# Performance work log

Measured on AMD Instinct MI355X. Metric: run time of the kernel, lower is better.

The kernel has to match this reference:

```python
import jax, jax.numpy as jnp
import numpy as np


def setup_inputs() -> dict:
    key = jax.random.key(0)
    ks = jax.random.split(key, 8)
    B, D, H, W = 4, 96, 64, 64
    K, N, R = 4, 16, 6
    return {
        "x": jax.random.normal(ks[0], (B, D, H, W), jnp.float32),
        "x_proj_weight": jax.random.normal(ks[1], (K, R + 2 * N, D), jnp.float32) * 0.05,
        "dt_projs_weight": jax.random.normal(ks[2], (K, D, R), jnp.float32) * 0.1,
        "dt_projs_bias": jax.random.normal(ks[3], (K, D), jnp.float32) * 0.1,
        "A_logs": jax.random.uniform(ks[4], (K * D, N), jnp.float32),
        "Ds": jax.random.normal(ks[5], (K * D,), jnp.float32),
        "ln_weight": jnp.ones((D,), jnp.float32),
        "ln_bias": jnp.zeros((D,), jnp.float32),
    }


def reference(x, x_proj_weight, dt_projs_weight, dt_projs_bias, A_logs, Ds, ln_weight, ln_bias):
    B, D, H, W = x.shape
    K, _, R = dt_projs_weight.shape
    N = A_logs.shape[1]
    L = H * W

    # ---- CrossScan: 4 traversal orders (row-major, col-major, and their reverses) ----
    xf = x.reshape(B, D, L)                                   # row-major
    xt = jnp.transpose(x, (0, 1, 3, 2)).reshape(B, D, L)      # col-major
    xs = jnp.stack([xf, xt, xf[..., ::-1], xt[..., ::-1]], axis=1)  # (B, K, D, L)

    # ---- input-dependent projections ----
    x_dbl = jnp.einsum('bkdl,kcd->bkcl', xs, x_proj_weight)   # (B, K, R+2N, L)
    dts, Bs, Cs = jnp.split(x_dbl, [R, R + N], axis=2)        # Bs/Cs: (B, K, N, L)
    dts = jnp.einsum('bkrl,kdr->bkdl', dts, dt_projs_weight)  # (B, K, D, L)

    A = -jnp.exp(A_logs).reshape(K, D, N)                     # (K, D, N)
    delta = jax.nn.softplus(dts + dt_projs_bias[None, :, :, None])  # (B, K, D, L)

    # ---- selective (S6) scan over L ----
    def step(h, inp):
        d_t, u_t, B_t, C_t = inp  # (B,K,D) (B,K,D) (B,K,N) (B,K,N)
        dA = jnp.exp(d_t[..., None] * A[None])                # (B,K,D,N)
        h = h * dA + (d_t * u_t)[..., None] * B_t[:, :, None, :]
        y_t = jnp.einsum('bkdn,bkn->bkd', h, C_t)
        return h, y_t

    h0 = jnp.zeros((B, K, D, N), x.dtype)
    seq = (jnp.moveaxis(delta, -1, 0), jnp.moveaxis(xs, -1, 0),
           jnp.moveaxis(Bs, -1, 0), jnp.moveaxis(Cs, -1, 0))
    _, ys = jax.lax.scan(step, h0, seq)                       # (L, B, K, D)
    ys = jnp.moveaxis(ys, 0, -1)                              # (B, K, D, L)
    ys = ys + Ds.reshape(K, D)[None, :, :, None] * xs         # skip term D*u

    # ---- CrossMerge: undo the 4 traversal orders and sum ----
    m = ys[:, 0:2] + ys[:, 2:4][..., ::-1]                    # (B, 2, D, L)
    y = m[:, 0] + jnp.transpose(m[:, 1].reshape(B, D, W, H), (0, 1, 3, 2)).reshape(B, D, L)

    # ---- out_norm (LayerNorm over channels, v0 path) ----
    y = jnp.transpose(y, (0, 2, 1))                           # (B, L, D)
    mu = y.mean(-1, keepdims=True)
    var = y.var(-1, keepdims=True)
    y = (y - mu) / jnp.sqrt(var + 1e-5) * ln_weight + ln_bias
    return y.reshape(B, H, W, D)
```

## Files before the change

### kernel.cpp

```cpp
#include <hip/hip_runtime.h>
#include <math.h>

#define B_ 4
#define D_ 96
#define H_ 64
#define W_ 64
#define L_ 4096
#define K_ 4
#define N_ 16
#define R_ 6
#define C_ 38
#define S_ 64
#define CL_ (L_ / S_)
#define CH_ (B_ * K_ * D_ * N_)

__device__ __forceinline__ int src_idx(int k, int l) {
    int m = (k >= 2) ? (L_ - 1 - l) : l;
    if (k & 1) {
        return ((m & 63) << 6) | (m >> 6);
    }
    return m;
}

__device__ __forceinline__ float softplus_f(float a) {
    return (a > 15.f) ? a : __logf(1.f + __expf(a));
}

__global__ __launch_bounds__(256) void proj_kernel(
    const float* __restrict__ x,
    const float* __restrict__ xpw,
    const float* __restrict__ wdt,
    const float* __restrict__ bdt,
    float* __restrict__ delta,
    float* __restrict__ xs_t,
    float* __restrict__ Bsb,
    float* __restrict__ Csb)
{
    const int TL = 64;
    const int tiles = L_ / TL;
    int bid = blockIdx.x;
    int bk = bid / tiles;
    int tile = bid % tiles;
    int b = bk / K_, k = bk % K_;
    int l0 = tile * TL;
    int tid = threadIdx.x;

    __shared__ __align__(16) float s_wpT[D_ * 40];
    __shared__ __align__(16) float s_xs[D_ * TL];
    __shared__ __align__(16) float s_wdt[R_ * D_];
    __shared__ __align__(16) float s_bias[D_];
    __shared__ __align__(16) float s_dts[R_ * 68];

    for (int i = tid; i < C_ * D_; i += 256) {
        int d = i / C_, c = i % C_;
        int cp = (c < 6) ? c : c + 2;
        s_wpT[d * 40 + cp] = xpw[(k * C_ + c) * D_ + d];
    }
    for (int i = tid; i < 96; i += 256) {
        s_wpT[i * 40 + 6] = 0.f;
        s_wpT[i * 40 + 7] = 0.f;
    }
    for (int i = tid; i < R_ * D_; i += 256) {
        int r = i / D_, d = i % D_;
        s_wdt[i] = wdt[(k * D_ + d) * R_ + r];
    }
    if (tid < D_) s_bias[tid] = bdt[k * D_ + tid];

    long base = (long)bk * L_ + l0;
    if (k & 1) {
        for (int i = tid; i < D_ * TL; i += 256) {
            int d = i >> 6, lt = i & 63;
            int src = (k == 1) ? (lt * 64 + tile) : ((63 - lt) * 64 + (63 - tile));
            s_xs[d * TL + lt] = x[(b * D_ + d) * L_ + src];
        }
    } else {
        for (int i = tid; i < D_ * 16; i += 256) {
            int d = i >> 4, q = i & 15;
            if (k == 0) {
                float4 v = *(const float4*)(x + (b * D_ + d) * L_ + l0 + q * 4);
                *(float4*)(&s_xs[d * TL + q * 4]) = v;
            } else {
                float4 v = *(const float4*)(x + (b * D_ + d) * L_ + (4092 - l0 - q * 4));
                *(float4*)(&s_xs[d * TL + q * 4]) = make_float4(v.w, v.z, v.y, v.x);
            }
        }
    }

    for (int i = tid; i < 24 * TL; i += 256) {
        int dq = i % 24, lt = i / 24;
        int d0 = dq * 4;
        int src = src_idx(k, l0 + lt);
        const float* xp = x + (long)b * D_ * L_ + src;
        float4 v = make_float4(xp[(d0 + 0) * L_], xp[(d0 + 1) * L_],
                               xp[(d0 + 2) * L_], xp[(d0 + 3) * L_]);
        *(float4*)(&xs_t[(base + lt) * D_ + d0]) = v;
    }
    __syncthreads();

    int ct = tid >> 4;
    int lt4 = (tid & 15) * 4;
    if (ct < 10) {
        int cp0 = ct * 4;
        float acc[4][4];
#pragma unroll
        for (int i = 0; i < 4; ++i)
#pragma unroll
            for (int j = 0; j < 4; ++j) acc[i][j] = 0.f;
#pragma unroll 4
        for (int d = 0; d < D_; ++d) {
            float4 wv = *(const float4*)(&s_wpT[d * 40 + cp0]);
            float4 xv = *(const float4*)(&s_xs[d * TL + lt4]);
            float wa[4] = {wv.x, wv.y, wv.z, wv.w};
            float xa[4] = {xv.x, xv.y, xv.z, xv.w};
#pragma unroll
            for (int ci = 0; ci < 4; ++ci)
#pragma unroll
                for (int li = 0; li < 4; ++li)
                    acc[ci][li] += wa[ci] * xa[li];
        }
        if (ct == 0) {
#pragma unroll
            for (int ci = 0; ci < 4; ++ci)
                *(float4*)(&s_dts[ci * 68 + lt4]) =
                    make_float4(acc[ci][0], acc[ci][1], acc[ci][2], acc[ci][3]);
        } else if (ct == 1) {
#pragma unroll
            for (int ci = 0; ci < 2; ++ci)
                *(float4*)(&s_dts[(4 + ci) * 68 + lt4]) =
                    make_float4(acc[ci][0], acc[ci][1], acc[ci][2], acc[ci][3]);
        } else if (ct < 6) {
            int n0 = cp0 - 8;
#pragma unroll
            for (int li = 0; li < 4; ++li)
                *(float4*)(&Bsb[(base + lt4 + li) * N_ + n0]) =
                    make_float4(acc[0][li], acc[1][li], acc[2][li], acc[3][li]);
        } else {
            int n0 = cp0 - 24;
#pragma unroll
            for (int li = 0; li < 4; ++li)
                *(float4*)(&Csb[(base + lt4 + li) * N_ + n0]) =
                    make_float4(acc[0][li], acc[1][li], acc[2][li], acc[3][li]);
        }
    }
    __syncthreads();

    for (int tt = tid; tt < 24 * 16; tt += 256) {
        int dt = tt % 24, lt4b = (tt / 24) * 4;
        int d0 = dt * 4;
        float4 bias = *(const float4*)(&s_bias[d0]);
        float acc[4][4];
#pragma unroll
        for (int li = 0; li < 4; ++li) {
            acc[li][0] = bias.x; acc[li][1] = bias.y;
            acc[li][2] = bias.z; acc[li][3] = bias.w;
        }
#pragma unroll
        for (int r = 0; r < R_; ++r) {
            float4 wv = *(const float4*)(&s_wdt[r * D_ + d0]);
            float4 tv = *(const float4*)(&s_dts[r * 68 + lt4b]);
            float wa[4] = {wv.x, wv.y, wv.z, wv.w};
            float ta[4] = {tv.x, tv.y, tv.z, tv.w};
#pragma unroll
            for (int li = 0; li < 4; ++li)
#pragma unroll
                for (int di = 0; di < 4; ++di)
                    acc[li][di] += ta[li] * wa[di];
        }
#pragma unroll
        for (int li = 0; li < 4; ++li) {
            float4 o = make_float4(softplus_f(acc[li][0]), softplus_f(acc[li][1]),
                                   softplus_f(acc[li][2]), softplus_f(acc[li][3]));
            *(float4*)(&delta[(base + lt4b + li) * D_ + d0]) = o;
        }
    }
}

__global__ __launch_bounds__(192) void scan_part1(
    const float* __restrict__ A_logs,
    const float* __restrict__ delta,
    const float* __restrict__ xs_t,
    const float* __restrict__ Bsb,
    float* __restrict__ pAarr,
    float* __restrict__ hharr)
{
    int bid = blockIdx.x;
    int bk = bid / S_;
    int j = bid % S_;
    int tid = threadIdx.x;
    int dd = tid >> 1;
    int half = tid & 1;
    int n0 = half * 8;
    int k = bk % K_;
    int kd = k * D_ + dd;
    int l0 = j * CL_;

    float Av[8];
    {
        const float4* ap = (const float4*)(A_logs + kd * N_ + n0);
        float4 a0 = ap[0], a1 = ap[1];
        Av[0] = -__expf(a0.x); Av[1] = -__expf(a0.y);
        Av[2] = -__expf(a0.z); Av[3] = -__expf(a0.w);
        Av[4] = -__expf(a1.x); Av[5] = -__expf(a1.y);
        Av[6] = -__expf(a1.z); Av[7] = -__expf(a1.w);
    }

    const float* dp = delta + ((long)bk * L_ + l0) * D_ + dd;
    const float* up = xs_t + ((long)bk * L_ + l0) * D_ + dd;
    const float* bp = Bsb + ((long)bk * L_ + l0) * N_ + n0;

    float h[8], pA[8];
#pragma unroll
    for (int i = 0; i < 8; ++i) { h[i] = 0.f; pA[i] = 1.f; }

#pragma unroll 4
    for (int t = 0; t < CL_; ++t) {
        float del = dp[t * D_];
        float u   = up[t * D_];
        float4 b0 = *(const float4*)(bp + t * N_);
        float4 b1 = *(const float4*)(bp + t * N_ + 4);
        float Bv[8] = {b0.x, b0.y, b0.z, b0.w, b1.x, b1.y, b1.z, b1.w};
        float delu = del * u;
#pragma unroll
        for (int i = 0; i < 8; ++i) {
            float dA = __expf(del * Av[i]);
            pA[i] *= dA;
            h[i] = h[i] * dA + delu * Bv[i];
        }
    }

    long sbase = (long)j * CH_ + (long)(bk * D_ + dd) * N_ + n0;
    *(float4*)(pAarr + sbase)     = make_float4(pA[0], pA[1], pA[2], pA[3]);
    *(float4*)(pAarr + sbase + 4) = make_float4(pA[4], pA[5], pA[6], pA[7]);
    *(float4*)(hharr + sbase)     = make_float4(h[0], h[1], h[2], h[3]);
    *(float4*)(hharr + sbase + 4) = make_float4(h[4], h[5], h[6], h[7]);
}

__global__ __launch_bounds__(256) void scan_combine(
    const float* __restrict__ pAarr,
    float* __restrict__ hharr)
{
    int c = blockIdx.x * 256 + threadIdx.x;
    float h = 0.f;
#pragma unroll 8
    for (int j = 0; j < S_; ++j) {
        long idx = (long)j * CH_ + c;
        float tmp = hharr[idx];
        float pa  = pAarr[idx];
        hharr[idx] = h;
        h = tmp + pa * h;
    }
}

__global__ __launch_bounds__(192) void scan_part2(
    const float* __restrict__ A_logs,
    const float* __restrict__ Ds,
    const float* __restrict__ delta,
    const float* __restrict__ xs_t,
    const float* __restrict__ Bsb,
    const float* __restrict__ Csb,
    const float* __restrict__ hharr,
    float* __restrict__ ys)
{
    int bid = blockIdx.x;
    int bk = bid / S_;
    int j = bid % S_;
    int tid = threadIdx.x;
    int dd = tid >> 1;
    int half = tid & 1;
    int n0 = half * 8;
    int k = bk % K_;
    int kd = k * D_ + dd;
    int l0 = j * CL_;

    float Av[8];
    {
        const float4* ap = (const float4*)(A_logs + kd * N_ + n0);
        float4 a0 = ap[0], a1 = ap[1];
        Av[0] = -__expf(a0.x); Av[1] = -__expf(a0.y);
        Av[2] = -__expf(a0.z); Av[3] = -__expf(a0.w);
        Av[4] = -__expf(a1.x); Av[5] = -__expf(a1.y);
        Av[6] = -__expf(a1.z); Av[7] = -__expf(a1.w);
    }
    float Dv = Ds[kd];

    const float* dp = delta + ((long)bk * L_ + l0) * D_ + dd;
    const float* up = xs_t + ((long)bk * L_ + l0) * D_ + dd;
    const float* bp = Bsb + ((long)bk * L_ + l0) * N_ + n0;
    const float* cp = Csb + ((long)bk * L_ + l0) * N_ + n0;
    float* yp = ys + ((long)bk * L_ + l0) * D_ + dd;

    float h[8];
    {
        long sbase = (long)j * CH_ + (long)(bk * D_ + dd) * N_ + n0;
        float4 h0 = *(const float4*)(hharr + sbase);
        float4 h1 = *(const float4*)(hharr + sbase + 4);
        h[0] = h0.x; h[1] = h0.y; h[2] = h0.z; h[3] = h0.w;
        h[4] = h1.x; h[5] = h1.y; h[6] = h1.z; h[7] = h1.w;
    }

#pragma unroll 4
    for (int t = 0; t < CL_; ++t) {
        float del = dp[t * D_];
        float u   = up[t * D_];
        float4 b0 = *(const float4*)(bp + t * N_);
        float4 b1 = *(const float4*)(bp + t * N_ + 4);
        float4 c0 = *(const float4*)(cp + t * N_);
        float4 c1 = *(const float4*)(cp + t * N_ + 4);
        float Bv[8] = {b0.x, b0.y, b0.z, b0.w, b1.x, b1.y, b1.z, b1.w};
        float Cv[8] = {c0.x, c0.y, c0.z, c0.w, c1.x, c1.y, c1.z, c1.w};
        float delu = del * u;
        float y = 0.f;
#pragma unroll
        for (int i = 0; i < 8; ++i) {
            float dA = __expf(del * Av[i]);
            h[i] = h[i] * dA + delu * Bv[i];
            y += h[i] * Cv[i];
        }
        y += __shfl_xor(y, 1);
        if (half == 0) yp[t * D_] = y + Dv * u;
    }
}

__global__ __launch_bounds__(64) void scan_serial(
    const float* __restrict__ x,
    const float* __restrict__ A_logs,
    const float* __restrict__ Ds,
    const float* __restrict__ delta,
    const float* __restrict__ Bsb,
    const float* __restrict__ Csb,
    float* __restrict__ ys)
{
    const int chans = D_ / 4;
    int bid = blockIdx.x;
    int bk = bid / chans;
    int d0 = (bid % chans) * 4;
    int b = bk / K_, k = bk % K_;
    int lane = threadIdx.x;
    int g = lane >> 4, n = lane & 15;
    int d = d0 + g;
    int kd = k * D_ + d;

    float A  = -__expf(A_logs[kd * N_ + n]);
    float Dv = Ds[kd];
    const float* dptr = delta + ((long)bk * L_) * D_ + d;
    const float* bptr = Bsb + (long)bk * L_ * N_ + n;
    const float* cptr = Csb + (long)bk * L_ * N_ + n;
    const float* xptr = x + ((long)b * D_ + d) * L_;
    float* yptr = ys + ((long)bk * L_) * D_ + d;

    float h = 0.f;
#pragma unroll 4
    for (int l = 0; l < L_; ++l) {
        float del = dptr[(long)l * D_];
        float u   = xptr[src_idx(k, l)];
        float Bt  = bptr[l * N_];
        float Ct  = cptr[l * N_];
        float dA  = __expf(del * A);
        h = h * dA + del * u * Bt;
        float yv = h * Ct;
        yv += __shfl_xor(yv, 1);
        yv += __shfl_xor(yv, 2);
        yv += __shfl_xor(yv, 4);
        yv += __shfl_xor(yv, 8);
        if (n == 0) yptr[(long)l * D_] = yv + Dv * u;
    }
}

__global__ __launch_bounds__(256) void merge_ln_kernel(
    const float* __restrict__ ys,
    const float* __restrict__ lnw,
    const float* __restrict__ lnb,
    float* __restrict__ out)
{
    int wid = (blockIdx.x * 256 + threadIdx.x) >> 6;
    int lane = threadIdx.x & 63;
    int b = wid / L_;
    int l = wid % L_;
    int lt = ((l & 63) << 6) | (l >> 6);

    long base0 = ((long)(b * K_ + 0) * L_ + l) * D_;
    long base2 = ((long)(b * K_ + 2) * L_ + (L_ - 1 - l)) * D_;
    long base1 = ((long)(b * K_ + 1) * L_ + lt) * D_;
    long base3 = ((long)(b * K_ + 3) * L_ + (L_ - 1 - lt)) * D_;

    int dA = lane;
    int dB = lane + 64;
    float v0 = ys[base0 + dA] + ys[base2 + dA] + ys[base1 + dA] + ys[base3 + dA];
    float v1 = 0.f;
    if (dB < D_)
        v1 = ys[base0 + dB] + ys[base2 + dB] + ys[base1 + dB] + ys[base3 + dB];

    float s  = v0 + v1;
    float s2 = v0 * v0 + v1 * v1;
#pragma unroll
    for (int m = 1; m < 64; m <<= 1) {
        s  += __shfl_xor(s, m);
        s2 += __shfl_xor(s2, m);
    }
    float mu  = s * (1.f / D_);
    float var = s2 * (1.f / D_) - mu * mu;
    float rstd = rsqrtf(var + 1e-5f);

    long obase = ((long)b * L_ + l) * D_;
    out[obase + dA] = (v0 - mu) * rstd * lnw[dA] + lnb[dA];
    if (dB < D_)
        out[obase + dB] = (v1 - mu) * rstd * lnw[dB] + lnb[dB];
}

extern "C" void kernel_launch(void* const* d_in, const int* in_sizes, int n_in,
                              void* d_out, int out_size, void* d_ws, size_t ws_size,
                              hipStream_t stream) {
    const float* x      = (const float*)d_in[0];
    const float* xpw    = (const float*)d_in[1];
    const float* wdt    = (const float*)d_in[2];
    const float* bdt    = (const float*)d_in[3];
    const float* A_logs = (const float*)d_in[4];
    const float* Ds     = (const float*)d_in[5];
    const float* lnw    = (const float*)d_in[6];
    const float* lnb    = (const float*)d_in[7];
    float* out = (float*)d_out;

    float* ws = (float*)d_ws;
    const long n_delta = (long)B_ * K_ * L_ * D_;
    const long n_bc    = (long)B_ * K_ * L_ * N_;
    const long n_sum   = (long)S_ * CH_;
    float* delta = ws;
    float* xs_t  = delta + n_delta;
    float* Bsb   = xs_t + n_delta;
    float* Csb   = Bsb + n_bc;
    float* ys    = Csb + n_bc;
    float* hharr = ys + n_delta;
    float* pAarr = ys;
    size_t need = (size_t)(n_delta * 3 + n_bc * 2 + n_sum) * sizeof(float);

    if (ws_size >= need) {
        proj_kernel<<<B_ * K_ * (L_ / 64), 256, 0, stream>>>(
            x, xpw, wdt, bdt, delta, xs_t, Bsb, Csb);
        scan_part1<<<B_ * K_ * S_, 192, 0, stream>>>(
            A_logs, delta, xs_t, Bsb, pAarr, hharr);
        scan_combine<<<CH_ / 256, 256, 0, stream>>>(pAarr, hharr);
        scan_part2<<<B_ * K_ * S_, 192, 0, stream>>>(
            A_logs, Ds, delta, xs_t, Bsb, Csb, hharr, ys);
        merge_ln_kernel<<<(B_ * L_) / 4, 256, 0, stream>>>(ys, lnw, lnb, out);
    } else {
        float* ys2 = Csb + n_bc;
        proj_kernel<<<B_ * K_ * (L_ / 64), 256, 0, stream>>>(
            x, xpw, wdt, bdt, delta, xs_t, Bsb, Csb);
        scan_serial<<<B_ * K_ * (D_ / 4), 64, 0, stream>>>(
            x, A_logs, Ds, delta, Bsb, Csb, ys2);
        merge_ln_kernel<<<(B_ * L_) / 4, 256, 0, stream>>>(ys2, lnw, lnb, out);
    }
}
```

Measured before the change: 198.2 us.

## Fuse cross-merge into scan via atomics, one thread per channel, more chunks

```diff
diff --git a/kernel.cpp b/kernel.cpp
--- a/kernel.cpp
+++ b/kernel.cpp
@@ -10,8 +10,6 @@
 #define N_ 16
 #define R_ 6
 #define C_ 38
-#define S_ 64
-#define CL_ (L_ / S_)
 #define CH_ (B_ * K_ * D_ * N_)
 
 __device__ __forceinline__ int src_idx(int k, int l) {
@@ -46,7 +44,7 @@
     int tid = threadIdx.x;
 
     __shared__ __align__(16) float s_wpT[D_ * 40];
-    __shared__ __align__(16) float s_xs[D_ * TL];
+    __shared__ __align__(16) float s_xs[D_ * 68];
     __shared__ __align__(16) float s_wdt[R_ * D_];
     __shared__ __align__(16) float s_bias[D_];
     __shared__ __align__(16) float s_dts[R_ * 68];
@@ -71,31 +69,29 @@
         for (int i = tid; i < D_ * TL; i += 256) {
             int d = i >> 6, lt = i & 63;
             int src = (k == 1) ? (lt * 64 + tile) : ((63 - lt) * 64 + (63 - tile));
-            s_xs[d * TL + lt] = x[(b * D_ + d) * L_ + src];
+            s_xs[d * 68 + lt] = x[(b * D_ + d) * L_ + src];
         }
     } else {
         for (int i = tid; i < D_ * 16; i += 256) {
             int d = i >> 4, q = i & 15;
             if (k == 0) {
                 float4 v = *(const float4*)(x + (b * D_ + d) * L_ + l0 + q * 4);
-                *(float4*)(&s_xs[d * TL + q * 4]) = v;
+                *(float4*)(&s_xs[d * 68 + q * 4]) = v;
             } else {
                 float4 v = *(const float4*)(x + (b * D_ + d) * L_ + (4092 - l0 - q * 4));
-                *(float4*)(&s_xs[d * TL + q * 4]) = make_float4(v.w, v.z, v.y, v.x);
+                *(float4*)(&s_xs[d * 68 + q * 4]) = make_float4(v.w, v.z, v.y, v.x);
             }
         }
     }
-
-    for (int i = tid; i < 24 * TL; i += 256) {
-        int dq = i % 24, lt = i / 24;
+    __syncthreads();
+
+    for (int idx = tid; idx < 24 * TL; idx += 256) {
+        int dq = idx % 24, lt = idx / 24;
         int d0 = dq * 4;
-        int src = src_idx(k, l0 + lt);
-        const float* xp = x + (long)b * D_ * L_ + src;
-        float4 v = make_float4(xp[(d0 + 0) * L_], xp[(d0 + 1) * L_],
-                               xp[(d0 + 2) * L_], xp[(d0 + 3) * L_]);
+        float4 v = make_float4(s_xs[(d0 + 0) * 68 + lt], s_xs[(d0 + 1) * 68 + lt],
+                               s_xs[(d0 + 2) * 68 + lt], s_xs[(d0 + 3) * 68 + lt]);
         *(float4*)(&xs_t[(base + lt) * D_ + d0]) = v;
     }
-    __syncthreads();
 
     int ct = tid >> 4;
     int lt4 = (tid & 15) * 4;
@@ -109,7 +105,7 @@
 #pragma unroll 4
         for (int d = 0; d < D_; ++d) {
             float4 wv = *(const float4*)(&s_wpT[d * 40 + cp0]);
-            float4 xv = *(const float4*)(&s_xs[d * TL + lt4]);
+            float4 xv = *(const float4*)(&s_xs[d * 68 + lt4]);
             float wa[4] = {wv.x, wv.y, wv.z, wv.w};
             float xa[4] = {xv.x, xv.y, xv.z, xv.w};
 #pragma unroll
@@ -175,6 +171,7 @@
     }
 }
 
+template <int SS>
 __global__ __launch_bounds__(192) void scan_part1(
     const float* __restrict__ A_logs,
     const float* __restrict__ delta,
@@ -183,58 +180,63 @@
     float* __restrict__ pAarr,
     float* __restrict__ hharr)
 {
-    int bid = blockIdx.x;
-    int bk = bid / S_;
-    int j = bid % S_;
-    int tid = threadIdx.x;
-    int dd = tid >> 1;
-    int half = tid & 1;
-    int n0 = half * 8;
+    constexpr int CLS = L_ / SS;
+    int cid = blockIdx.x * 2 + threadIdx.x / 96;
+    int dd = threadIdx.x % 96;
+    int bk = cid / SS;
+    int j = cid % SS;
     int k = bk % K_;
     int kd = k * D_ + dd;
-    int l0 = j * CL_;
-
-    float Av[8];
+    int l0 = j * CLS;
+
+    float Av[16];
     {
-        const float4* ap = (const float4*)(A_logs + kd * N_ + n0);
-        float4 a0 = ap[0], a1 = ap[1];
-        Av[0] = -__expf(a0.x); Av[1] = -__expf(a0.y);
-        Av[2] = -__expf(a0.z); Av[3] = -__expf(a0.w);
-        Av[4] = -__expf(a1.x); Av[5] = -__expf(a1.y);
-        Av[6] = -__expf(a1.z); Av[7] = -__expf(a1.w);
+        const float4* ap = (const float4*)(A_logs + kd * N_);
+#pragma unroll
+        for (int q = 0; q < 4; ++q) {
+            float4 a = ap[q];
+            Av[q * 4 + 0] = -__expf(a.x); Av[q * 4 + 1] = -__expf(a.y);
+            Av[q * 4 + 2] = -__expf(a.z); Av[q * 4 + 3] = -__expf(a.w);
+        }
     }
 
     const float* dp = delta + ((long)bk * L_ + l0) * D_ + dd;
     const float* up = xs_t + ((long)bk * L_ + l0) * D_ + dd;
-    const float* bp = Bsb + ((long)bk * L_ + l0) * N_ + n0;
-
-    float h[8], pA[8];
-#pragma unroll
-    for (int i = 0; i < 8; ++i) { h[i] = 0.f; pA[i] = 1.f; }
-
-#pragma unroll 4
-    for (int t = 0; t < CL_; ++t) {
+    const float* bp = Bsb + ((long)bk * L_ + l0) * N_;
+
+    float h[16], pA[16];
+#pragma unroll
+    for (int i = 0; i < 16; ++i) { h[i] = 0.f; pA[i] = 1.f; }
+
+#pragma unroll 2
+    for (int t = 0; t < CLS; ++t) {
         float del = dp[t * D_];
         float u   = up[t * D_];
-        float4 b0 = *(const float4*)(bp + t * N_);
-        float4 b1 = *(const float4*)(bp + t * N_ + 4);
-        float Bv[8] = {b0.x, b0.y, b0.z, b0.w, b1.x, b1.y, b1.z, b1.w};
+        float Bv[16];
+        *(float4*)(Bv + 0)  = *(const float4*)(bp + t * N_);
+        *(float4*)(Bv + 4)  = *(const float4*)(bp + t * N_ + 4);
+        *(float4*)(Bv + 8)  = *(const float4*)(bp + t * N_ + 8);
+        *(float4*)(Bv + 12) = *(const float4*)(bp + t * N_ + 12);
         float delu = del * u;
 #pragma unroll
-        for (int i = 0; i < 8; ++i) {
+        for (int i = 0; i < 16; ++i) {
             float dA = __expf(del * Av[i]);
             pA[i] *= dA;
             h[i] = h[i] * dA + delu * Bv[i];
         }
     }
 
-    long sbase = (long)j * CH_ + (long)(bk * D_ + dd) * N_ + n0;
-    *(float4*)(pAarr + sbase)     = make_float4(pA[0], pA[1], pA[2], pA[3]);
-    *(float4*)(pAarr + sbase + 4) = make_float4(pA[4], pA[5], pA[6], pA[7]);
-    *(float4*)(hharr + sbase)     = make_float4(h[0], h[1], h[2], h[3]);
-    *(float4*)(hharr + sbase + 4) = make_float4(h[4], h[5], h[6], h[7]);
-}
-
+    long sbase = (long)j * CH_ + (long)(bk * D_ + dd) * N_;
+#pragma unroll
+    for (int q = 0; q < 4; ++q) {
+        *(float4*)(pAarr + sbase + q * 4) =
+            make_float4(pA[q * 4], pA[q * 4 + 1], pA[q * 4 + 2], pA[q * 4 + 3]);
+        *(float4*)(hharr + sbase + q * 4) =
+            make_float4(h[q * 4], h[q * 4 + 1], h[q * 4 + 2], h[q * 4 + 3]);
+    }
+}
+
+template <int SS>
 __global__ __launch_bounds__(256) void scan_combine(
     const float* __restrict__ pAarr,
     float* __restrict__ hharr)
@@ -242,7 +244,7 @@
     int c = blockIdx.x * 256 + threadIdx.x;
     float h = 0.f;
 #pragma unroll 8
-    for (int j = 0; j < S_; ++j) {
+    for (int j = 0; j < SS; ++j) {
         long idx = (long)j * CH_ + c;
         float tmp = hharr[idx];
         float pa  = pAarr[idx];
@@ -251,6 +253,7 @@
     }
 }
 
+template <int SS>
 __global__ __launch_bounds__(192) void scan_part2(
     const float* __restrict__ A_logs,
     const float* __restrict__ Ds,
@@ -259,66 +262,98 @@
     const float* __restrict__ Bsb,
     const float* __restrict__ Csb,
     const float* __restrict__ hharr,
-    float* __restrict__ ys)
-{
-    int bid = blockIdx.x;
-    int bk = bid / S_;
-    int j = bid % S_;
-    int tid = threadIdx.x;
-    int dd = tid >> 1;
-    int half = tid & 1;
-    int n0 = half * 8;
-    int k = bk % K_;
+    float* __restrict__ y)
+{
+    constexpr int CLS = L_ / SS;
+    int cid = blockIdx.x * 2 + threadIdx.x / 96;
+    int dd = threadIdx.x % 96;
+    int bk = cid / SS;
+    int j = cid % SS;
+    int b = bk / K_, k = bk % K_;
     int kd = k * D_ + dd;
-    int l0 = j * CL_;
-
-    float Av[8];
+    int l0 = j * CLS;
+
+    float Av[16];
     {
-        const float4* ap = (const float4*)(A_logs + kd * N_ + n0);
-        float4 a0 = ap[0], a1 = ap[1];
-        Av[0] = -__expf(a0.x); Av[1] = -__expf(a0.y);
-        Av[2] = -__expf(a0.z); Av[3] = -__expf(a0.w);
-        Av[4] = -__expf(a1.x); Av[5] = -__expf(a1.y);
-        Av[6] = -__expf(a1.z); Av[7] = -__expf(a1.w);
+        const float4* ap = (const float4*)(A_logs + kd * N_);
+#pragma unroll
+        for (int q = 0; q < 4; ++q) {
+            float4 a = ap[q];
+            Av[q * 4 + 0] = -__expf(a.x); Av[q * 4 + 1] = -__expf(a.y);
+            Av[q * 4 + 2] = -__expf(a.z); Av[q * 4 + 3] = -__expf(a.w);
+        }
     }
     float Dv = Ds[kd];
 
     const float* dp = delta + ((long)bk * L_ + l0) * D_ + dd;
     const float* up = xs_t + ((long)bk * L_ + l0) * D_ + dd;
-    const float* bp = Bsb + ((long)bk * L_ + l0) * N_ + n0;
-    const float* cp = Csb + ((long)bk * L_ + l0) * N_ + n0;
-    float* yp = ys + ((long)bk * L_ + l0) * D_ + dd;
-
-    float h[8];
+    const float* bp = Bsb + ((long)bk * L_ + l0) * N_;
+    const float* cp = Csb + ((long)bk * L_ + l0) * N_;
+
+    float h[16];
     {
-        long sbase = (long)j * CH_ + (long)(bk * D_ + dd) * N_ + n0;
-        float4 h0 = *(const float4*)(hharr + sbase);
-        float4 h1 = *(const float4*)(hharr + sbase + 4);
-        h[0] = h0.x; h[1] = h0.y; h[2] = h0.z; h[3] = h0.w;
-        h[4] = h1.x; h[5] = h1.y; h[6] = h1.z; h[7] = h1.w;
-    }
-
-#pragma unroll 4
-    for (int t = 0; t < CL_; ++t) {
+        long sbase = (long)j * CH_ + (long)(bk * D_ + dd) * N_;
+#pragma unroll
+        for (int q = 0; q < 4; ++q) {
+            float4 hv = *(const float4*)(hharr + sbase + q * 4);
+            h[q * 4] = hv.x; h[q * 4 + 1] = hv.y; h[q * 4 + 2] = hv.z; h[q * 4 + 3] = hv.w;
+        }
+    }
+
+    float* ybase = y + (long)b * L_ * D_ + dd;
+#pragma unroll 2
+    for (int t = 0; t < CLS; ++t) {
         float del = dp[t * D_];
         float u   = up[t * D_];
-        float4 b0 = *(const float4*)(bp + t * N_);
-        float4 b1 = *(const float4*)(bp + t * N_ + 4);
-        float4 c0 = *(const float4*)(cp + t * N_);
-        float4 c1 = *(const float4*)(cp + t * N_ + 4);
-        float Bv[8] = {b0.x, b0.y, b0.z, b0.w, b1.x, b1.y, b1.z, b1.w};
-        float Cv[8] = {c0.x, c0.y, c0.z, c0.w, c1.x, c1.y, c1.z, c1.w};
+        float Bv[16], Cv[16];
+        *(float4*)(Bv + 0)  = *(const float4*)(bp + t * N_);
+        *(float4*)(Bv + 4)  = *(const float4*)(bp + t * N_ + 4);
+        *(float4*)(Bv + 8)  = *(const float4*)(bp + t * N_ + 8);
+        *(float4*)(Bv + 12) = *(const float4*)(bp + t * N_ + 12);
+        *(float4*)(Cv + 0)  = *(const float4*)(cp + t * N_);
+        *(float4*)(Cv + 4)  = *(const float4*)(cp + t * N_ + 4);
+        *(float4*)(Cv + 8)  = *(const float4*)(cp + t * N_ + 8);
+        *(float4*)(Cv + 12) = *(const float4*)(cp + t * N_ + 12);
         float delu = del * u;
-        float y = 0.f;
-#pragma unroll
-        for (int i = 0; i < 8; ++i) {
+        float yv = 0.f;
+#pragma unroll
+        for (int i = 0; i < 16; ++i) {
             float dA = __expf(del * Av[i]);
             h[i] = h[i] * dA + delu * Bv[i];
-            y += h[i] * Cv[i];
-        }
-        y += __shfl_xor(y, 1);
-        if (half == 0) yp[t * D_] = y + Dv * u;
-    }
+            yv += h[i] * Cv[i];
+        }
+        int sidx = src_idx(k, l0 + t);
+        atomicAdd(ybase + (long)sidx * D_, yv + Dv * u);
+    }
+}
+
+__global__ __launch_bounds__(256) void ln_kernel(
+    const float* __restrict__ y,
+    const float* __restrict__ lnw,
+    const float* __restrict__ lnb,
+    float* __restrict__ out)
+{
+    int wid = (blockIdx.x * 256 + threadIdx.x) >> 6;
+    int lane = threadIdx.x & 63;
+    long base = (long)wid * D_;
+
+    float v0 = y[base + lane];
+    float v1 = (lane < 32) ? y[base + 64 + lane] : 0.f;
+
+    float s  = v0 + v1;
+    float s2 = v0 * v0 + v1 * v1;
+#pragma unroll
+    for (int m = 1; m < 64; m <<= 1) {
+        s  += __shfl_xor(s, m);
+        s2 += __shfl_xor(s2, m);
+    }
+    float mu  = s * (1.f / D_);
+    float var = s2 * (1.f / D_) - mu * mu;
+    float rstd = rsqrtf(var + 1e-5f);
+
+    out[base + lane] = (v0 - mu) * rstd * lnw[lane] + lnb[lane];
+    if (lane < 32)
+        out[base + 64 + lane] = (v1 - mu) * rstd * lnw[64 + lane] + lnb[64 + lane];
 }
 
 __global__ __launch_bounds__(64) void scan_serial(
@@ -423,27 +458,41 @@
     float* ws = (float*)d_ws;
     const long n_delta = (long)B_ * K_ * L_ * D_;
     const long n_bc    = (long)B_ * K_ * L_ * N_;
-    const long n_sum   = (long)S_ * CH_;
+    const long n_y     = (long)B_ * L_ * D_;
+
     float* delta = ws;
     float* xs_t  = delta + n_delta;
     float* Bsb   = xs_t + n_delta;
     float* Csb   = Bsb + n_bc;
-    float* ys    = Csb + n_bc;
-    float* hharr = ys + n_delta;
-    float* pAarr = ys;
-    size_t need = (size_t)(n_delta * 3 + n_bc * 2 + n_sum) * sizeof(float);
-
-    if (ws_size >= need) {
+    float* yb    = Csb + n_bc;
+    float* pAarr = yb + n_y;
+    size_t need128 = (size_t)(2 * n_delta + 2 * n_bc + n_y + 2L * 128 * CH_) * 4;
+    size_t need64  = (size_t)(2 * n_delta + 2 * n_bc + n_y + 2L * 64 * CH_) * 4;
+
+    if (ws_size >= need64) {
         proj_kernel<<<B_ * K_ * (L_ / 64), 256, 0, stream>>>(
             x, xpw, wdt, bdt, delta, xs_t, Bsb, Csb);
-        scan_part1<<<B_ * K_ * S_, 192, 0, stream>>>(
-            A_logs, delta, xs_t, Bsb, pAarr, hharr);
-        scan_combine<<<CH_ / 256, 256, 0, stream>>>(pAarr, hharr);
-        scan_part2<<<B_ * K_ * S_, 192, 0, stream>>>(
-            A_logs, Ds, delta, xs_t, Bsb, Csb, hharr, ys);
-        merge_ln_kernel<<<(B_ * L_) / 4, 256, 0, stream>>>(ys, lnw, lnb, out);
+        hipMemsetAsync(yb, 0, n_y * sizeof(float), stream);
+        if (ws_size >= need128) {
+            const int SS = 128;
+            float* hharr = pAarr + (long)SS * CH_;
+            scan_part1<SS><<<B_ * K_ * SS / 2, 192, 0, stream>>>(
+                A_logs, delta, xs_t, Bsb, pAarr, hharr);
+            scan_combine<SS><<<CH_ / 256, 256, 0, stream>>>(pAarr, hharr);
+            scan_part2<SS><<<B_ * K_ * SS / 2, 192, 0, stream>>>(
+                A_logs, Ds, delta, xs_t, Bsb, Csb, hharr, yb);
+        } else {
+            const int SS = 64;
+            float* hharr = pAarr + (long)SS * CH_;
+            scan_part1<SS><<<B_ * K_ * SS / 2, 192, 0, stream>>>(
+                A_logs, delta, xs_t, Bsb, pAarr, hharr);
+            scan_combine<SS><<<CH_ / 256, 256, 0, stream>>>(pAarr, hharr);
+            scan_part2<SS><<<B_ * K_ * SS / 2, 192, 0, stream>>>(
+                A_logs, Ds, delta, xs_t, Bsb, Csb, hharr, yb);
+        }
+        ln_kernel<<<(B_ * L_) / 4, 256, 0, stream>>>(yb, lnw, lnb, out);
     } else {
-        float* ys2 = Csb + n_bc;
+        float* ys2 = xs_t;
         proj_kernel<<<B_ * K_ * (L_ / 64), 256, 0, stream>>>(
             x, xpw, wdt, bdt, delta, xs_t, Bsb, Csb);
         scan_serial<<<B_ * K_ * (D_ / 4), 64, 0, stream>>>(
```

Result: slower. 236.7 us (+19.4%).
